# Kernel tuning notes

Measured on AMD Instinct MI355X. Metric: run time of the kernel, lower is better.

## Reference

```python
import jax, jax.numpy as jnp
import numpy as np

N_TYPES = 4
N_DESC = 8
K_MAX = 8
R_C = 5.0
L_MAX = 4
N_ATOMS = 10000
M_NBR = 20


def chebyshev_basis(r, r_c, k_max):
    fc = jnp.where(r < r_c, 0.5 * jnp.cos(jnp.pi * r / r_c) + 0.5, jnp.zeros_like(r))
    x = 2.0 * (r / r_c - 1.0) ** 2 - 1.0
    fn = [jnp.ones_like(x), x]
    for _ in range(2, k_max):
        fn.append(2.0 * x * fn[-1] - fn[-2])
    fn = jnp.stack(fn[:k_max], axis=-1)  # [T, k_max]
    return (fn + 1.0) * (0.5 * fc)[..., None]


def legendre_basis(cos_theta, l_max):
    pl = [jnp.ones_like(cos_theta), cos_theta]
    for l in range(2, l_max):
        pl.append(((2 * l - 1) * cos_theta * pl[-1] - (l - 1) * pl[-2]) / l)
    return jnp.stack(pl[:l_max], axis=-1)  # [T, l_max]


def setup_inputs() -> dict:
    key = jax.random.key(0)
    k1, k2, k3, k4 = jax.random.split(key, 4)
    types = jax.random.randint(k1, (N_ATOMS,), 0, N_TYPES)
    # small box so pair distances mostly fall under the cutoff r_c
    positions = jax.random.uniform(k2, (N_ATOMS, 3), dtype=jnp.float32) * 4.0
    # all neighbor slots valid (no -1 padding) and never the atom itself
    offs = jax.random.randint(k3, (N_ATOMS, M_NBR), 1, N_ATOMS)
    angular_neighbors = (jnp.arange(N_ATOMS)[:, None] + offs) % N_ATOMS
    c_table = jax.random.normal(k4, (N_TYPES, N_TYPES, N_DESC, K_MAX), dtype=jnp.float32)
    return {"types": types, "positions": positions,
            "angular_neighbors": angular_neighbors, "c_table": c_table}


def reference(types, positions, angular_neighbors, c_table):
    N, M = angular_neighbors.shape
    ju, ku = np.triu_indices(M, 1)  # P = M*(M-1)//2 pairs per atom
    P = ju.shape[0]
    j_idx = angular_neighbors[:, ju].reshape(-1)  # [N*P]
    k_idx = angular_neighbors[:, ku].reshape(-1)
    i_idx = jnp.repeat(jnp.arange(N), P)

    pos_i = positions[i_idx]
    rij = positions[j_idx] - pos_i
    rik = positions[k_idx] - pos_i
    r_ij = jnp.linalg.norm(rij, axis=-1)
    r_ik = jnp.linalg.norm(rik, axis=-1)
    cos_theta = jnp.sum(rij * rik, axis=-1) / (r_ij * r_ik + 1e-8)

    type_i = types[i_idx]
    f_ij = chebyshev_basis(r_ij, R_C, K_MAX)  # [T, k]
    f_ik = chebyshev_basis(r_ik, R_C, K_MAX)
    c_ij = c_table[type_i, types[j_idx]]  # [T, n_desc, k]
    c_ik = c_table[type_i, types[k_idx]]
    g_ij = jnp.einsum('tdk,tk->td', c_ij, f_ij)  # [T, n_desc]
    g_ik = jnp.einsum('tdk,tk->td', c_ik, f_ik)

    P_l = legendre_basis(cos_theta, L_MAX)  # [T, l_max]
    ang = (g_ij * g_ik)[:, :, None] * P_l[:, None, :]  # [T, n_desc, l_max]
    q = jax.ops.segment_sum(ang, i_idx, num_segments=N)  # [N, n_desc, l_max]
    return q
```

## Files before the change

### kernel.cpp

```cpp
#include <hip/hip_runtime.h>

#define N_TYPES 4
#define N_DESC  8
#define K_MAX   8
#define M_NBR   20
#define NCOMP   20
#define ATOMS   16
#define BLOCK   256
#define P1_ITEMS (ATOMS * M_NBR)

constexpr float R_C = 5.0f;
constexpr float SQ2 = 1.41421356237309515f;
constexpr float SQ3 = 1.73205080756887729f;
constexpr float SQ6 = 2.44948974968163702f;

__global__ __launch_bounds__(BLOCK) void AngularDescriptor_kernel(
    const int*   __restrict__ types,
    const float* __restrict__ pos,
    const int*   __restrict__ nbr,
    const float* __restrict__ c_table,
    float*       __restrict__ out,
    int N)
{
    __shared__ float sF[ATOMS][M_NBR][NCOMP];
    __shared__ float sg[ATOMS][N_DESC][M_NBR];

    const int t     = threadIdx.x;
    const int atom0 = blockIdx.x * ATOMS;

    for (int e = t; e < P1_ITEMS; e += BLOCK) {
        const int a    = e / M_NBR;
        const int m    = e - a * M_NBR;
        const int atom = atom0 + a;
        if (atom < N) {
            const int j  = nbr[atom * M_NBR + m];
            const int ti = types[atom];
            const int tj = types[j];
            const float dx = pos[j * 3 + 0] - pos[atom * 3 + 0];
            const float dy = pos[j * 3 + 1] - pos[atom * 3 + 1];
            const float dz = pos[j * 3 + 2] - pos[atom * 3 + 2];
            const float r2   = dx * dx + dy * dy + dz * dz;
            const float rinv = __builtin_amdgcn_rsqf(r2);
            const float r    = r2 * rinv;

            const float fc  = (r < R_C)
                ? (0.5f * __builtin_amdgcn_cosf(r * (0.5f / R_C)) + 0.5f) : 0.0f;
            const float hfc = 0.5f * fc;
            const float u   = r * (1.0f / R_C) - 1.0f;
            const float x   = 2.0f * u * u - 1.0f;
            float ch[K_MAX];
            ch[0] = 2.0f * hfc;
            ch[1] = (x + 1.0f) * hfc;
            float tkm2 = 1.0f, tkm1 = x;
            #pragma unroll
            for (int k = 2; k < K_MAX; ++k) {
                const float tk = 2.0f * x * tkm1 - tkm2;
                ch[k] = (tk + 1.0f) * hfc;
                tkm2 = tkm1; tkm1 = tk;
            }

            const float* crow = c_table + (ti * N_TYPES + tj) * (N_DESC * K_MAX);
            float g[N_DESC];
            #pragma unroll
            for (int d = 0; d < N_DESC; ++d) {
                const float4 c0 = ((const float4*)crow)[2 * d + 0];
                const float4 c1 = ((const float4*)crow)[2 * d + 1];
                g[d] = c0.x * ch[0] + c0.y * ch[1] + c0.z * ch[2] + c0.w * ch[3]
                     + c1.x * ch[4] + c1.y * ch[5] + c1.z * ch[6] + c1.w * ch[7];
            }
            #pragma unroll
            for (int dd = 0; dd < N_DESC; ++dd) {
                const int d = (dd + a) & 7;
                sg[a][d][m] = g[d];
            }

            const float ux = dx * rinv, uy = dy * rinv, uz = dz * rinv;
            const float x2 = ux * ux, y2 = uy * uy, z2 = uz * uz;
            float F[NCOMP];
            F[0]  = 1.0f;
            F[1]  = ux;  F[2] = uy;  F[3] = uz;
            F[4]  = x2 - (1.0f / 3.0f);
            F[5]  = y2 - (1.0f / 3.0f);
            F[6]  = z2 - (1.0f / 3.0f);
            F[7]  = SQ2 * ux * uy;
            F[8]  = SQ2 * ux * uz;
            F[9]  = SQ2 * uy * uz;
            F[10] = ux * (x2 - 0.6f);
            F[11] = uy * (y2 - 0.6f);
            F[12] = uz * (z2 - 0.6f);
            F[13] = SQ3 * uy * (x2 - 0.2f);
            F[14] = SQ3 * uz * (x2 - 0.2f);
            F[15] = SQ3 * ux * (y2 - 0.2f);
            F[16] = SQ3 * uz * (y2 - 0.2f);
            F[17] = SQ3 * ux * (z2 - 0.2f);
            F[18] = SQ3 * uy * (z2 - 0.2f);
            F[19] = SQ6 * ux * uy * uz;
            float4* frow = (float4*)&sF[a][m][0];
            const int mr = m % 5;
            #pragma unroll
            for (int ss = 0; ss < 5; ++ss) {
                int cc = ss + mr; cc = (cc >= 5) ? cc - 5 : cc;
                frow[cc] = make_float4(F[4*cc+0], F[4*cc+1], F[4*cc+2], F[4*cc+3]);
            }
        }
    }
    __syncthreads();

    if (t < ATOMS * N_DESC) {
        const int a    = t >> 3;
        const int d    = t & 7;
        const int atom = atom0 + a;
        if (atom < N) {
            float g[M_NBR];
            const float4* gr = (const float4*)&sg[a][d][0];
            #pragma unroll
            for (int i = 0; i < 5; ++i) {
                const float4 v = gr[i];
                g[4*i+0] = v.x; g[4*i+1] = v.y; g[4*i+2] = v.z; g[4*i+3] = v.w;
            }
            float G2 = 0.f;
            #pragma unroll
            for (int m = 0; m < M_NBR; ++m) G2 = fmaf(g[m], g[m], G2);

            float acc[NCOMP];
            #pragma unroll
            for (int c = 0; c < NCOMP; ++c) acc[c] = 0.f;
            #pragma unroll
            for (int m = 0; m < M_NBR; ++m) {
                const float4* Fr = (const float4*)&sF[a][m][0];
                const float gm = g[m];
                #pragma unroll
                for (int i = 0; i < 5; ++i) {
                    const float4 f = Fr[i];
                    acc[4*i+0] = fmaf(gm, f.x, acc[4*i+0]);
                    acc[4*i+1] = fmaf(gm, f.y, acc[4*i+1]);
                    acc[4*i+2] = fmaf(gm, f.z, acc[4*i+2]);
                    acc[4*i+3] = fmaf(gm, f.w, acc[4*i+3]);
                }
            }
            float p1 = acc[1]*acc[1] + acc[2]*acc[2] + acc[3]*acc[3];
            float p2 = 0.f, p3 = 0.f;
            #pragma unroll
            for (int c = 4; c < 10; ++c)  p2 = fmaf(acc[c], acc[c], p2);
            #pragma unroll
            for (int c = 10; c < 20; ++c) p3 = fmaf(acc[c], acc[c], p3);
            const float hG2 = 0.5f * G2;
            ((float4*)out)[atom * N_DESC + d] = make_float4(
                0.5f  * acc[0] * acc[0] - hG2,
                0.5f  * p1               - hG2,
                0.75f * p2               - hG2,
                1.25f * p3               - hG2);
        }
    }
}

extern "C" void kernel_launch(void* const* d_in, const int* in_sizes, int n_in,
                              void* d_out, int out_size, void* d_ws, size_t ws_size,
                              hipStream_t stream) {
    const int*   types   = (const int*)  d_in[0];
    const float* pos     = (const float*)d_in[1];
    const int*   nbr     = (const int*)  d_in[2];
    const float* c_table = (const float*)d_in[3];
    float*       out     = (float*)      d_out;

    const int N = in_sizes[0];
    const int grid = (N + ATOMS - 1) / ATOMS;
    AngularDescriptor_kernel<<<grid, BLOCK, 0, stream>>>(types, pos, nbr, c_table, out, N);
}
```

Before: 73.40 us.

## Shrink blocks to one wavefront with two atoms and split contraction across lanes

Each block now handles 2 atoms with 64 threads, one wavefront, instead of 16 atoms with 256 threads. Shared arrays are transposed to a component-major layout with padded rows of 28. The second phase gives each (atom, descriptor) pair 4 lanes, each computing 5 of the 20 harmonic components, and combines the l-channel sums with xor shuffles. The aim is to use all lanes in phase 2, where the old code kept half the threads idle, and to cut per-thread register pressure. The cost is 5000 small blocks, so more launch and scheduling overhead per unit of work, 24 of 64 lanes idle in phase 1, and scalar strided LDS stores.

Result: faster. 66.04 us (-10.0%).

```diff
diff --git a/kernel.cpp b/kernel.cpp
--- a/kernel.cpp
+++ b/kernel.cpp
@@ -5,16 +5,15 @@
 #define K_MAX   8
 #define M_NBR   20
 #define NCOMP   20
-#define ATOMS   16
-#define BLOCK   256
-#define P1_ITEMS (ATOMS * M_NBR)
+#define APB     2
+#define ROWP    28
 
 constexpr float R_C = 5.0f;
 constexpr float SQ2 = 1.41421356237309515f;
 constexpr float SQ3 = 1.73205080756887729f;
 constexpr float SQ6 = 2.44948974968163702f;
 
-__global__ __launch_bounds__(BLOCK) void AngularDescriptor_kernel(
+__global__ __launch_bounds__(64) void AngularDescriptor_kernel(
     const int*   __restrict__ types,
     const float* __restrict__ pos,
     const int*   __restrict__ nbr,
@@ -22,15 +21,15 @@
     float*       __restrict__ out,
     int N)
 {
-    __shared__ float sF[ATOMS][M_NBR][NCOMP];
-    __shared__ float sg[ATOMS][N_DESC][M_NBR];
+    __shared__ float sF[APB][NCOMP][ROWP];
+    __shared__ float sg[APB][N_DESC][ROWP];
 
     const int t     = threadIdx.x;
-    const int atom0 = blockIdx.x * ATOMS;
+    const int atom0 = blockIdx.x * APB;
 
-    for (int e = t; e < P1_ITEMS; e += BLOCK) {
-        const int a    = e / M_NBR;
-        const int m    = e - a * M_NBR;
+    if (t < APB * M_NBR) {
+        const int a    = (t >= M_NBR) ? 1 : 0;
+        const int m    = t - a * M_NBR;
         const int atom = atom0 + a;
         if (atom < N) {
             const int j  = nbr[atom * M_NBR + m];
@@ -60,18 +59,12 @@
             }
 
             const float* crow = c_table + (ti * N_TYPES + tj) * (N_DESC * K_MAX);
-            float g[N_DESC];
             #pragma unroll
             for (int d = 0; d < N_DESC; ++d) {
                 const float4 c0 = ((const float4*)crow)[2 * d + 0];
                 const float4 c1 = ((const float4*)crow)[2 * d + 1];
-                g[d] = c0.x * ch[0] + c0.y * ch[1] + c0.z * ch[2] + c0.w * ch[3]
-                     + c1.x * ch[4] + c1.y * ch[5] + c1.z * ch[6] + c1.w * ch[7];
-            }
-            #pragma unroll
-            for (int dd = 0; dd < N_DESC; ++dd) {
-                const int d = (dd + a) & 7;
-                sg[a][d][m] = g[d];
+                sg[a][d][m] = c0.x * ch[0] + c0.y * ch[1] + c0.z * ch[2] + c0.w * ch[3]
+                            + c1.x * ch[4] + c1.y * ch[5] + c1.z * ch[6] + c1.w * ch[7];
             }
 
             const float ux = dx * rinv, uy = dy * rinv, uz = dz * rinv;
@@ -95,61 +88,63 @@
             F[17] = SQ3 * ux * (z2 - 0.2f);
             F[18] = SQ3 * uy * (z2 - 0.2f);
             F[19] = SQ6 * ux * uy * uz;
-            float4* frow = (float4*)&sF[a][m][0];
-            const int mr = m % 5;
             #pragma unroll
-            for (int ss = 0; ss < 5; ++ss) {
-                int cc = ss + mr; cc = (cc >= 5) ? cc - 5 : cc;
-                frow[cc] = make_float4(F[4*cc+0], F[4*cc+1], F[4*cc+2], F[4*cc+3]);
-            }
+            for (int c = 0; c < NCOMP; ++c) sF[a][c][m] = F[c];
         }
     }
     __syncthreads();
 
-    if (t < ATOMS * N_DESC) {
-        const int a    = t >> 3;
-        const int d    = t & 7;
+    {
+        const int a    = t >> 5;
+        const int d    = (t >> 2) & 7;
+        const int q    = t & 3;
         const int atom = atom0 + a;
         if (atom < N) {
-            float g[M_NBR];
             const float4* gr = (const float4*)&sg[a][d][0];
+            const float4 g0 = gr[0], g1 = gr[1], g2 = gr[2], g3 = gr[3], g4 = gr[4];
+            float G2 = g0.x*g0.x + g0.y*g0.y + g0.z*g0.z + g0.w*g0.w
+                     + g1.x*g1.x + g1.y*g1.y + g1.z*g1.z + g1.w*g1.w
+                     + g2.x*g2.x + g2.y*g2.y + g2.z*g2.z + g2.w*g2.w
+                     + g3.x*g3.x + g3.y*g3.y + g3.z*g3.z + g3.w*g3.w
+                     + g4.x*g4.x + g4.y*g4.y + g4.z*g4.z + g4.w*g4.w;
+
+            float A[5];
             #pragma unroll
             for (int i = 0; i < 5; ++i) {
-                const float4 v = gr[i];
-                g[4*i+0] = v.x; g[4*i+1] = v.y; g[4*i+2] = v.z; g[4*i+3] = v.w;
+                const int c = 4 * i + q;
+                const float4* Fr = (const float4*)&sF[a][c][0];
+                const float4 f0 = Fr[0], f1 = Fr[1], f2 = Fr[2], f3 = Fr[3], f4 = Fr[4];
+                A[i] = g0.x*f0.x + g0.y*f0.y + g0.z*f0.z + g0.w*f0.w
+                     + g1.x*f1.x + g1.y*f1.y + g1.z*f1.z + g1.w*f1.w
+                     + g2.x*f2.x + g2.y*f2.y + g2.z*f2.z + g2.w*f2.w
+                     + g3.x*f3.x + g3.y*f3.y + g3.z*f3.z + g3.w*f3.w
+                     + g4.x*f4.x + g4.y*f4.y + g4.z*f4.z + g4.w*f4.w;
             }
-            float G2 = 0.f;
+
+            float Px = 0.f, Py = 0.f, Pz = 0.f, Pw = 0.f;
+            {
+                const float v = 0.5f * A[0] * A[0];
+                if (q == 0) Px = v; else Py = v;
+            }
+            Pz += 0.75f * A[1] * A[1];
+            {
+                const float v = A[2] * A[2];
+                if (q < 2) Pz += 0.75f * v; else Pw += 1.25f * v;
+            }
+            Pw += 1.25f * A[3] * A[3];
+            Pw += 1.25f * A[4] * A[4];
+
             #pragma unroll
-            for (int m = 0; m < M_NBR; ++m) G2 = fmaf(g[m], g[m], G2);
+            for (int off = 1; off <= 2; off <<= 1) {
+                Px += __shfl_xor(Px, off, 64);
+                Py += __shfl_xor(Py, off, 64);
+                Pz += __shfl_xor(Pz, off, 64);
+                Pw += __shfl_xor(Pw, off, 64);
+            }
 
-            float acc[NCOMP];
-            #pragma unroll
-            for (int c = 0; c < NCOMP; ++c) acc[c] = 0.f;
-            #pragma unroll
-            for (int m = 0; m < M_NBR; ++m) {
-                const float4* Fr = (const float4*)&sF[a][m][0];
-                const float gm = g[m];
-                #pragma unroll
-                for (int i = 0; i < 5; ++i) {
-                    const float4 f = Fr[i];
-                    acc[4*i+0] = fmaf(gm, f.x, acc[4*i+0]);
-                    acc[4*i+1] = fmaf(gm, f.y, acc[4*i+1]);
-                    acc[4*i+2] = fmaf(gm, f.z, acc[4*i+2]);
-                    acc[4*i+3] = fmaf(gm, f.w, acc[4*i+3]);
-                }
-            }
-            float p1 = acc[1]*acc[1] + acc[2]*acc[2] + acc[3]*acc[3];
-            float p2 = 0.f, p3 = 0.f;
-            #pragma unroll
-            for (int c = 4; c < 10; ++c)  p2 = fmaf(acc[c], acc[c], p2);
-            #pragma unroll
-            for (int c = 10; c < 20; ++c) p3 = fmaf(acc[c], acc[c], p3);
-            const float hG2 = 0.5f * G2;
-            ((float4*)out)[atom * N_DESC + d] = make_float4(
-                0.5f  * acc[0] * acc[0] - hG2,
-                0.5f  * p1               - hG2,
-                0.75f * p2               - hG2,
-                1.25f * p3               - hG2);
+            const float v01 = (q & 1) ? Py : Px;
+            const float v23 = (q & 1) ? Pw : Pz;
+            out[atom0 * 32 + t] = ((q & 2) ? v23 : v01) - 0.5f * G2;
         }
     }
 }
@@ -164,6 +159,6 @@
     float*       out     = (float*)      d_out;
 
     const int N = in_sizes[0];
-    const int grid = (N + ATOMS - 1) / ATOMS;
-    AngularDescriptor_kernel<<<grid, BLOCK, 0, stream>>>(types, pos, nbr, c_table, out, N);
+    const int grid = (N + APB - 1) / APB;
+    AngularDescriptor_kernel<<<grid, 64, 0, stream>>>(types, pos, nbr, c_table, out, N);
 }
```
